# Optimization experiments

Measured on AMD Instinct MI355X. Metric: run time of the kernel, lower is better.

Reference implementation:

```python
import jax, jax.numpy as jnp
import numpy as np

N = 65536   # number of GP locations
M = 64      # max ancestor set size (contiguous window A(i) = {i-M+1..i})
B = 16384   # minibatch size


def setup_inputs() -> dict:
    rng = np.random.default_rng(0)
    i = np.arange(N)
    # CSR row lengths: U (lower-tri) row i has cols {max(0,i-M+1)..i}; V (upper-tri) row j has cols {j..min(j+M-1,N-1)}
    row_len_u = np.minimum(i + 1, M)
    row_len_v = np.minimum(M, N - i)
    crow_u = np.concatenate([[0], np.cumsum(row_len_u)]).astype(np.int32)
    crow_v = np.concatenate([[0], np.cumsum(row_len_v)]).astype(np.int32)
    nnz = int(crow_u[-1])  # 4192288, same for both matrices
    # off-diagonals small, diagonals near 1 (kept positive for logDet and solve stability)
    U_values = (rng.standard_normal(nnz) * 0.1).astype(np.float32)
    U_values[crow_u[1:] - 1] = rng.uniform(0.8, 1.2, N).astype(np.float32)  # last entry of row i = (i,i)
    V_values = (rng.standard_normal(nnz) * 0.1).astype(np.float32)
    V_values[crow_v[:-1]] = rng.uniform(0.8, 1.2, N).astype(np.float32)    # first entry of row i = (i,i)
    mean = (rng.standard_normal(N) * 0.5).astype(np.float32)
    mean_post = (rng.standard_normal(N) * 0.5).astype(np.float32)
    y = rng.standard_normal(N).astype(np.float32)
    mini_indices = rng.integers(0, N, B).astype(np.int32)
    return {
        'U_values': jnp.asarray(U_values),
        'V_values': jnp.asarray(V_values),
        'mean': jnp.asarray(mean),
        'mean_post': jnp.asarray(mean_post),
        'y': jnp.asarray(y),
        'noise': jnp.float32(0.1),
        'mini_indices': jnp.asarray(mini_indices),
        'crow_u': jnp.asarray(crow_u),
        'crow_v': jnp.asarray(crow_v),
    }


def reference(U_values, V_values, mean, mean_post, y, noise, mini_indices, crow_u, crow_v):
    nnz = U_values.shape[0]
    g = mini_indices                       # [B] selected rows
    L = jnp.minimum(g + 1, M)              # n_anc per selected row
    p = jnp.arange(M)
    valid = p[None, :] >= (M - L)[:, None]                 # [B,M] right-aligned validity mask
    anc = g[:, None] - (M - 1 - p)[None, :]                # global ancestor index at padded slot p
    anc_c = jnp.clip(anc, 0, N - 1)

    # get_sub_rows(UTrans): row g entries at A(g), right-aligned into [B,M]
    u_idx = crow_u[g][:, None] + (p[None, :] - (M - L)[:, None])
    U_sub = jnp.where(valid, U_values[jnp.clip(u_idx, 0, nnz - 1)], 0.0)

    # ragged mean difference gather (masked scatter in the original)
    md = jnp.where(valid, (mean - mean_post)[anc_c], 0.0)  # [B,M]

    # get_sub_mat(V, unit_diag=True): V[A(g),A(g)] bottom-right aligned, identity padding
    jrow = anc_c[:, :, None]                               # global row index of block row r
    icol = anc_c[:, None, :]                               # global col index of block col c
    vidx = crow_v[jrow] + (icol - jrow)                    # CSR value index of V[jrow, icol]
    blk_mask = (valid[:, :, None] & valid[:, None, :]
                & (p[None, :, None] <= p[None, None, :]))  # upper-tri of active block
    eye = jnp.eye(M, dtype=U_values.dtype)
    V_sub = jnp.where(blk_mask, V_values[jnp.clip(vidx, 0, nnz - 1)], eye[None, :, :])  # [B,M,M]

    # batched triangular solves
    ej = jnp.zeros((B, M), U_values.dtype).at[:, -1].set(1.0)
    sol_e = jax.scipy.linalg.solve_triangular(V_sub, ej[:, :, None], lower=False)
    marginalVarPost = jnp.sum(sol_e * sol_e, axis=(1, 2))  # [B]
    sol_u = jax.scipy.linalg.solve_triangular(V_sub, U_sub[:, :, None], lower=False)
    innerCov = -0.5 * jnp.sum(sol_u * sol_u)

    innerMean = -0.5 * jnp.sum(jnp.sum(U_sub * md, axis=1) ** 2)

    # log-determinant terms from diagonal gathers
    logDet = (jnp.sum(jnp.log(U_values[crow_u[g + 1] - 1]))
              - jnp.sum(jnp.log(V_values[crow_v[g]])))

    # Gaussian expected likelihood (noise is not None branch)
    resid = y[g] - mean_post[g]
    ell = (-0.5 * B * jnp.log(2.0 * jnp.pi * noise)
           - (jnp.sum(resid * resid) + jnp.sum(marginalVarPost)) / (2.0 * noise))

    return logDet + innerMean + innerCov + ell
```

## Files before the change

kernel.cpp:

```cpp
#include <hip/hip_runtime.h>
#include <math.h>

constexpr int kN = 65536;
constexpr int kB = 16384;
constexpr int kTileW = 2560;

static __device__ __forceinline__ float bcastf(float v, int lane) {
    union { float f; int i; } u;
    u.f = v;
    u.i = __builtin_amdgcn_readlane(u.i, lane);
    return u.f;
}

static __device__ __forceinline__ void gload_lds16(const float* g, float* l) {
    __builtin_amdgcn_global_load_lds(
        (const __attribute__((address_space(1))) void*)g,
        (__attribute__((address_space(3))) void*)l, 16, 0, 0);
}
static __device__ __forceinline__ void gload_lds4(const float* g, float* l) {
    __builtin_amdgcn_global_load_lds(
        (const __attribute__((address_space(1))) void*)g,
        (__attribute__((address_space(3))) void*)l, 4, 0, 0);
}

static __device__ __forceinline__ int row_start(int j) {
    const int t = j >> 4;
    return 1024 * t - 128 * t * (t - 1) + (64 - 16 * t) * (j - 16 * t);
}

static __device__ __forceinline__ bool is_hot(int g) {
    return (g >= 63) && (g <= kN - 63);
}

__global__ __launch_bounds__(64) void gp_solve_kernel(
    const float* __restrict__ Uv,
    const float* __restrict__ Vv,
    const float* __restrict__ mean,
    const float* __restrict__ mean_post,
    const float* __restrict__ y,
    const int*   __restrict__ gidx,
    const int*   __restrict__ crow_u,
    const int*   __restrict__ crow_v,
    const float* __restrict__ noise,
    float*       __restrict__ partial)
{
    __shared__ __align__(16) float myl[kTileW];

    const int lane = (int)threadIdx.x;
    const int b    = (int)blockIdx.x;
    const int g    = gidx[b];

    const int  anc = g - 63 + lane;
    const bool vl  = (anc >= 0);

    const int L  = (g + 1 < 64) ? (g + 1) : 64;
    const int ub = (g >= 63) ? (2016 + 64 * (g - 63)) : crow_u[g];

    float uval = 0.0f, md = 0.0f;
    if (vl) {
        uval = Uv[ub + lane - (64 - L)];
        md   = mean[anc] - mean_post[anc];
    }
    const float yg  = y[g];
    const float mpg = mean_post[g];

    if (is_hot(g)) {
        const float* base = Vv + 64 * (g - 63);
        {
            const float* src = base + 4 * lane;
            #pragma unroll
            for (int k = 0; k < 4; ++k)
                gload_lds16(src + 256 * k, myl + 256 * k);
        }
        #pragma unroll
        for (int k = 0; k < 3; ++k) {
            const int w   = 256 * k + 4 * lane;
            const int jj  = ((w >> 4) * 171) >> 9;
            const int col = w - 48 * jj;
            gload_lds16(base + 64 * (16 + jj) + col, myl + 1024 + 256 * k);
        }
        #pragma unroll
        for (int k = 0; k < 2; ++k) {
            const int w = 256 * k + 4 * lane;
            gload_lds16(base + 64 * (32 + (w >> 5)) + (w & 31), myl + 1792 + 256 * k);
        }
        {
            const int w = 4 * lane;
            gload_lds16(base + 64 * (48 + (w >> 4)) + (w & 15), myl + 2304);
        }
    } else {
        int rowbase = 0;
        if (vl) rowbase = crow_v[anc];
        for (int j = 0; j < 64; ++j) {
            const int rbj = __builtin_amdgcn_readlane(rowbase, j);
            const int dst = row_start(j);
            if (lane < 64 - j) {
                if (g - 63 + j >= 0)
                    gload_lds4(Vv + rbj + lane, myl + dst);
                else
                    myl[dst + lane] = 0.0f;
            }
        }
    }
    asm volatile("s_waitcnt vmcnt(0) lgkmcnt(0)" ::: "memory");

    const int rs = row_start(lane);
    const float d0   = myl[rs];
    const float diag = vl ? d0 : 1.0f;
    const float invd = 1.0f / diag;

    const float* vrow = myl + (rs - lane);
    float v[64];
    #pragma unroll
    for (int i = 0; i < 64; i += 2) {
        const float a0 = vrow[i];
        const float a1 = vrow[i + 1];
        v[i]     = a0 * invd;
        v[i + 1] = a1 * invd;
    }

    float r_e = (lane == 63) ? invd : 0.0f;
    float r_u = uval * invd;
    float acc_e = 0.0f, acc_u = 0.0f;

    #pragma unroll
    for (int i = 63; i >= 0; --i) {
        const float s_e = bcastf(r_e, i);
        const float s_u = bcastf(r_u, i);
        r_e = fmaf(-v[i], s_e, r_e);
        r_u = fmaf(-v[i], s_u, r_u);
        acc_e = fmaf(s_e, s_e, acc_e);
        acc_u = fmaf(s_u, s_u, acc_u);
    }

    float dot = uval * md;
    #pragma unroll
    for (int m = 1; m < 64; m <<= 1)
        dot += __shfl_xor(dot, m, 64);

    const float ulast  = bcastf(uval, 63);
    const float vfirst = bcastf(diag, 63);

    if (lane == 0) {
        const float resid = yg - mpg;
        const float inv2n = 0.5f / noise[0];
        partial[b] = __logf(ulast) - __logf(vfirst)
                   - 0.5f * dot * dot
                   - 0.5f * acc_u
                   - (resid * resid + acc_e) * inv2n;
    }
}

__global__ __launch_bounds__(1024) void gp_reduce_kernel(
    const float* __restrict__ partial,
    const float* __restrict__ noise,
    float*       __restrict__ out)
{
    __shared__ float ws[16];
    const int t = (int)threadIdx.x;
    float a = 0.0f;
    #pragma unroll
    for (int k = 0; k < 4; ++k) {
        const float4 p = reinterpret_cast<const float4*>(partial)[t + 1024 * k];
        a += (p.x + p.y) + (p.z + p.w);
    }
    #pragma unroll
    for (int m = 1; m < 64; m <<= 1)
        a += __shfl_xor(a, m, 64);
    if ((t & 63) == 0) ws[t >> 6] = a;
    __syncthreads();
    if (t == 0) {
        float tot = 0.0f;
        #pragma unroll
        for (int k = 0; k < 16; ++k) tot += ws[k];
        tot += -0.5f * (float)kB * logf(2.0f * 3.14159265358979323846f * noise[0]);
        out[0] = tot;
    }
}

extern "C" void kernel_launch(void* const* d_in, const int* in_sizes, int n_in,
                              void* d_out, int out_size, void* d_ws, size_t ws_size,
                              hipStream_t stream)
{
    const float* Uv        = (const float*)d_in[0];
    const float* Vv        = (const float*)d_in[1];
    const float* mean      = (const float*)d_in[2];
    const float* mean_post = (const float*)d_in[3];
    const float* y         = (const float*)d_in[4];
    const float* noise     = (const float*)d_in[5];
    const int*   gidx      = (const int*)d_in[6];
    const int*   crow_u    = (const int*)d_in[7];
    const int*   crow_v    = (const int*)d_in[8];
    float* partial = (float*)d_ws;

    gp_solve_kernel<<<dim3(kB), dim3(64), 0, stream>>>(
        Uv, Vv, mean, mean_post, y, gidx, crow_u, crow_v, noise, partial);
    gp_reduce_kernel<<<dim3(1), dim3(1024), 0, stream>>>(
        partial, noise, (float*)d_out);
}
```

Baseline: 36.94 us.

## Bucket-sort minibatch rows and swizzle block order for L2 locality

Adds a counting sort of the minibatch indices into 1024 buckets of 64 rows each, using a histogram, a scan and an atomic scatter. The solve kernel then reads its row from the sorted order, with a block-id swizzle that spreads contiguous sorted ranges across the 8 XCDs. The goal is for blocks whose V windows overlap to run close together on the same XCD so those V tile loads hit in L2. The cost is four extra small kernel launches and their atomics. Because the scatter order is nondeterministic, the summation order of the partials also becomes nondeterministic.

```diff
diff --git a/kernel.cpp b/kernel.cpp
--- a/kernel.cpp
+++ b/kernel.cpp
@@ -4,6 +4,7 @@
 constexpr int kN = 65536;
 constexpr int kB = 16384;
 constexpr int kTileW = 2560;
+constexpr int kBuckets = 1024;
 
 static __device__ __forceinline__ float bcastf(float v, int lane) {
     union { float f; int i; } u;
@@ -31,6 +32,50 @@
 static __device__ __forceinline__ bool is_hot(int g) {
     return (g >= 63) && (g <= kN - 63);
 }
+
+
+__global__ __launch_bounds__(1024) void gp_zero_hist(int* __restrict__ hist) {
+    hist[threadIdx.x] = 0;
+}
+
+__global__ __launch_bounds__(1024) void gp_hist_kernel(
+    const int* __restrict__ gidx, int* __restrict__ hist)
+{
+    const int i = (int)blockIdx.x * 1024 + (int)threadIdx.x;
+    atomicAdd(&hist[gidx[i] >> 6], 1);
+}
+
+__global__ __launch_bounds__(1024) void gp_scan_kernel(
+    const int* __restrict__ hist, int* __restrict__ base)
+{
+    __shared__ int wsum[16];
+    const int t = (int)threadIdx.x, lane = t & 63, w = t >> 6;
+    const int v = hist[t];
+    int x = v;
+    #pragma unroll
+    for (int d = 1; d < 64; d <<= 1) {
+        const int n = __shfl_up(x, d, 64);
+        if (lane >= d) x += n;
+    }
+    if (lane == 63) wsum[w] = x;
+    __syncthreads();
+    if (t == 0) {
+        int acc = 0;
+        #pragma unroll
+        for (int k = 0; k < 16; ++k) { const int s = wsum[k]; wsum[k] = acc; acc += s; }
+    }
+    __syncthreads();
+    base[t] = x - v + wsum[w];
+}
+
+__global__ __launch_bounds__(1024) void gp_scatter_kernel(
+    const int* __restrict__ gidx, int* __restrict__ base, int* __restrict__ sorted)
+{
+    const int i = (int)blockIdx.x * 1024 + (int)threadIdx.x;
+    const int pos = atomicAdd(&base[gidx[i] >> 6], 1);
+    sorted[pos] = i;
+}
+
 
 __global__ __launch_bounds__(64) void gp_solve_kernel(
     const float* __restrict__ Uv,
@@ -42,12 +87,15 @@
     const int*   __restrict__ crow_u,
     const int*   __restrict__ crow_v,
     const float* __restrict__ noise,
+    const int*   __restrict__ sorted,
     float*       __restrict__ partial)
 {
     __shared__ __align__(16) float myl[kTileW];
 
     const int lane = (int)threadIdx.x;
-    const int b    = (int)blockIdx.x;
+    const int bid  = (int)blockIdx.x;
+    const int slot = ((bid & 7) << 11) | (bid >> 3);
+    const int b    = sorted[slot];
     const int g    = gidx[b];
 
     const int  anc = g - 63 + lane;
@@ -144,10 +192,10 @@
     if (lane == 0) {
         const float resid = yg - mpg;
         const float inv2n = 0.5f / noise[0];
-        partial[b] = __logf(ulast) - __logf(vfirst)
-                   - 0.5f * dot * dot
-                   - 0.5f * acc_u
-                   - (resid * resid + acc_e) * inv2n;
+        partial[slot] = __logf(ulast) - __logf(vfirst)
+                      - 0.5f * dot * dot
+                      - 0.5f * acc_u
+                      - (resid * resid + acc_e) * inv2n;
     }
 }
 
@@ -191,10 +239,20 @@
     const int*   gidx      = (const int*)d_in[6];
     const int*   crow_u    = (const int*)d_in[7];
     const int*   crow_v    = (const int*)d_in[8];
-    float* partial = (float*)d_ws;
+
+    int*   ws_i    = (int*)d_ws;
+    int*   sorted  = ws_i;
+    int*   hist    = ws_i + kB;
+    int*   base    = ws_i + kB + kBuckets;
+    float* partial = (float*)(ws_i + kB + 2 * kBuckets);
+
+    gp_zero_hist   <<<dim3(1),       dim3(1024), 0, stream>>>(hist);
+    gp_hist_kernel <<<dim3(kB/1024), dim3(1024), 0, stream>>>(gidx, hist);
+    gp_scan_kernel <<<dim3(1),       dim3(1024), 0, stream>>>(hist, base);
+    gp_scatter_kernel<<<dim3(kB/1024), dim3(1024), 0, stream>>>(gidx, base, sorted);
 
     gp_solve_kernel<<<dim3(kB), dim3(64), 0, stream>>>(
-        Uv, Vv, mean, mean_post, y, gidx, crow_u, crow_v, noise, partial);
+        Uv, Vv, mean, mean_post, y, gidx, crow_u, crow_v, noise, sorted, partial);
     gp_reduce_kernel<<<dim3(1), dim3(1024), 0, stream>>>(
         partial, noise, (float*)d_out);
 }
```

Measured after the change: 48.15 us. 30.3% more time.

## Process eight samples per wave with double-buffered LDS prefetch

Applied to the files above, without the earlier changes.

Each 64-thread block now handles eight minibatch rows instead of one. It uses two LDS buffers so the async global-to-LDS load of the next sample's V block, U row and means overlaps the triangular solve of the current one, with partial vmcnt waits on the hot path. This cuts block count and launch overhead, hides memory latency inside a wave, and makes the final reduction read one float4 per thread. The trade-off is less parallelism across blocks (2048 waves), more LDS per block, and correctness that depends on the hand-counted vmcnt(13) wait being right.

```diff
diff --git a/kernel.cpp b/kernel.cpp
--- a/kernel.cpp
+++ b/kernel.cpp
@@ -3,7 +3,13 @@
 
 constexpr int kN = 65536;
 constexpr int kB = 16384;
+constexpr int kEPB = 8;
+constexpr int kBlocks = kB / kEPB;
 constexpr int kTileW = 2560;
+constexpr int kAuxU = 2560;
+constexpr int kAuxM = 2624;
+constexpr int kAuxP = 2688;
+constexpr int kBufW = 2752;
 
 static __device__ __forceinline__ float bcastf(float v, int lane) {
     union { float f; int i; } u;
@@ -23,6 +29,8 @@
         (__attribute__((address_space(3))) void*)l, 4, 0, 0);
 }
 
+#define CB() asm volatile("" ::: "memory")
+
 static __device__ __forceinline__ int row_start(int j) {
     const int t = j >> 4;
     return 1024 * t - 128 * t * (t - 1) + (64 - 16 * t) * (j - 16 * t);
@@ -31,6 +39,123 @@
 static __device__ __forceinline__ bool is_hot(int g) {
     return (g >= 63) && (g <= kN - 63);
 }
+
+static __device__ __forceinline__ void stage_one(
+    int g, int lane, float* buf,
+    const float* __restrict__ Uv, const float* __restrict__ Vv,
+    const float* __restrict__ mean, const float* __restrict__ mean_post,
+    const int* __restrict__ crow_u, const int* __restrict__ crow_v)
+{
+    if (is_hot(g)) {
+        const float* base = Vv + 64 * (g - 63);
+        {
+            const float* src = base + 4 * lane;
+            #pragma unroll
+            for (int k = 0; k < 4; ++k)
+                gload_lds16(src + 256 * k, buf + 256 * k);
+        }
+        #pragma unroll
+        for (int k = 0; k < 3; ++k) {
+            const int w   = 256 * k + 4 * lane;
+            const int jj  = ((w >> 4) * 171) >> 9;
+            const int col = w - 48 * jj;
+            gload_lds16(base + 64 * (16 + jj) + col, buf + 1024 + 256 * k);
+        }
+        #pragma unroll
+        for (int k = 0; k < 2; ++k) {
+            const int w = 256 * k + 4 * lane;
+            gload_lds16(base + 64 * (32 + (w >> 5)) + (w & 31), buf + 1792 + 256 * k);
+        }
+        {
+            const int w = 4 * lane;
+            gload_lds16(base + 64 * (48 + (w >> 4)) + (w & 15), buf + 2304);
+        }
+        const int ub = 2016 + 64 * (g - 63);
+        gload_lds4(Uv + ub + lane,               buf + kAuxU);
+        gload_lds4(mean + (g - 63) + lane,       buf + kAuxM);
+        gload_lds4(mean_post + (g - 63) + lane,  buf + kAuxP);
+    } else {
+        const int  anc = g - 63 + lane;
+        const bool vl  = (anc >= 0);
+        const int  L   = (g + 1 < 64) ? (g + 1) : 64;
+        const int  ub  = crow_u[g];
+        for (int j = 0; j < 64; ++j) {
+            if ((g - 63 + j) < 0 && lane < 64 - j)
+                buf[row_start(j) + lane] = 0.0f;
+        }
+        buf[kAuxU + lane] = 0.0f;
+        buf[kAuxM + lane] = 0.0f;
+        buf[kAuxP + lane] = 0.0f;
+        asm volatile("s_waitcnt lgkmcnt(0)" ::: "memory");
+        int rowbase = 0;
+        if (vl) rowbase = crow_v[anc];
+        for (int j = 0; j < 64; ++j) {
+            const int rbj = __builtin_amdgcn_readlane(rowbase, j);
+            if ((g - 63 + j) >= 0 && lane < 64 - j)
+                gload_lds4(Vv + rbj + lane, buf + row_start(j));
+        }
+        if (vl) {
+            gload_lds4(Uv + ub + lane - (64 - L), buf + kAuxU);
+            gload_lds4(mean + anc,                buf + kAuxM);
+            gload_lds4(mean_post + anc,           buf + kAuxP);
+        }
+    }
+}
+
+static __device__ __forceinline__ float compute_one(
+    int g, int lane, const float* buf, float inv2n)
+{
+    const int  anc = g - 63 + lane;
+    const bool vl  = (anc >= 0);
+
+    const int rs = row_start(lane);
+    const float d0   = buf[rs];
+    const float diag = vl ? d0 : 1.0f;
+    const float invd = 1.0f / diag;
+
+    const float uval = buf[kAuxU + lane];
+    const float md   = buf[kAuxM + lane] - buf[kAuxP + lane];
+
+    const float* vrow = buf + (rs - lane);
+    float v[64];
+    #pragma unroll
+    for (int i = 0; i < 64; i += 2) {
+        const float a0 = vrow[i];
+        const float a1 = vrow[i + 1];
+        v[i]     = a0 * invd;
+        v[i + 1] = a1 * invd;
+    }
+
+    float r_e = (lane == 63) ? invd : 0.0f;
+    float r_u = uval * invd;
+    float acc_e = 0.0f, acc_u = 0.0f;
+
+    #pragma unroll
+    for (int i = 63; i >= 0; --i) {
+        const float s_e = bcastf(r_e, i);
+        const float s_u = bcastf(r_u, i);
+        r_e = fmaf(-v[i], s_e, r_e);
+        r_u = fmaf(-v[i], s_u, r_u);
+        acc_e = fmaf(s_e, s_e, acc_e);
+        acc_u = fmaf(s_u, s_u, acc_u);
+    }
+
+    float dot = uval * md;
+    #pragma unroll
+    for (int m = 1; m < 64; m <<= 1)
+        dot += __shfl_xor(dot, m, 64);
+
+    const float ulast  = bcastf(uval, 63);
+    const float vfirst = bcastf(diag, 63);
+
+    return __logf(ulast) - __logf(vfirst)
+         - 0.5f * dot * dot
+         - 0.5f * acc_u
+         - acc_e * inv2n;
+}
+
+#define WAIT_HOT()  asm volatile("s_waitcnt vmcnt(13) lgkmcnt(0)" ::: "memory")
+#define WAIT_ALL()  asm volatile("s_waitcnt vmcnt(0)  lgkmcnt(0)" ::: "memory")
 
 __global__ __launch_bounds__(64) void gp_solve_kernel(
     const float* __restrict__ Uv,
@@ -44,126 +169,70 @@
     const float* __restrict__ noise,
     float*       __restrict__ partial)
 {
-    __shared__ __align__(16) float myl[kTileW];
-
-    const int lane = (int)threadIdx.x;
-    const int b    = (int)blockIdx.x;
-    const int g    = gidx[b];
-
-    const int  anc = g - 63 + lane;
-    const bool vl  = (anc >= 0);
-
-    const int L  = (g + 1 < 64) ? (g + 1) : 64;
-    const int ub = (g >= 63) ? (2016 + 64 * (g - 63)) : crow_u[g];
-
-    float uval = 0.0f, md = 0.0f;
-    if (vl) {
-        uval = Uv[ub + lane - (64 - L)];
-        md   = mean[anc] - mean_post[anc];
-    }
-    const float yg  = y[g];
-    const float mpg = mean_post[g];
-
-    if (is_hot(g)) {
-        const float* base = Vv + 64 * (g - 63);
-        {
-            const float* src = base + 4 * lane;
-            #pragma unroll
-            for (int k = 0; k < 4; ++k)
-                gload_lds16(src + 256 * k, myl + 256 * k);
-        }
-        #pragma unroll
-        for (int k = 0; k < 3; ++k) {
-            const int w   = 256 * k + 4 * lane;
-            const int jj  = ((w >> 4) * 171) >> 9;
-            const int col = w - 48 * jj;
-            gload_lds16(base + 64 * (16 + jj) + col, myl + 1024 + 256 * k);
-        }
-        #pragma unroll
-        for (int k = 0; k < 2; ++k) {
-            const int w = 256 * k + 4 * lane;
-            gload_lds16(base + 64 * (32 + (w >> 5)) + (w & 31), myl + 1792 + 256 * k);
-        }
-        {
-            const int w = 4 * lane;
-            gload_lds16(base + 64 * (48 + (w >> 4)) + (w & 15), myl + 2304);
-        }
-    } else {
-        int rowbase = 0;
-        if (vl) rowbase = crow_v[anc];
-        for (int j = 0; j < 64; ++j) {
-            const int rbj = __builtin_amdgcn_readlane(rowbase, j);
-            const int dst = row_start(j);
-            if (lane < 64 - j) {
-                if (g - 63 + j >= 0)
-                    gload_lds4(Vv + rbj + lane, myl + dst);
-                else
-                    myl[dst + lane] = 0.0f;
-            }
-        }
-    }
-    asm volatile("s_waitcnt vmcnt(0) lgkmcnt(0)" ::: "memory");
-
-    const int rs = row_start(lane);
-    const float d0   = myl[rs];
-    const float diag = vl ? d0 : 1.0f;
-    const float invd = 1.0f / diag;
-
-    const float* vrow = myl + (rs - lane);
-    float v[64];
-    #pragma unroll
-    for (int i = 0; i < 64; i += 2) {
-        const float a0 = vrow[i];
-        const float a1 = vrow[i + 1];
-        v[i]     = a0 * invd;
-        v[i + 1] = a1 * invd;
-    }
-
-    float r_e = (lane == 63) ? invd : 0.0f;
-    float r_u = uval * invd;
-    float acc_e = 0.0f, acc_u = 0.0f;
-
-    #pragma unroll
-    for (int i = 63; i >= 0; --i) {
-        const float s_e = bcastf(r_e, i);
-        const float s_u = bcastf(r_u, i);
-        r_e = fmaf(-v[i], s_e, r_e);
-        r_u = fmaf(-v[i], s_u, r_u);
-        acc_e = fmaf(s_e, s_e, acc_e);
-        acc_u = fmaf(s_u, s_u, acc_u);
-    }
-
-    float dot = uval * md;
-    #pragma unroll
-    for (int m = 1; m < 64; m <<= 1)
-        dot += __shfl_xor(dot, m, 64);
-
-    const float ulast  = bcastf(uval, 63);
-    const float vfirst = bcastf(diag, 63);
-
-    if (lane == 0) {
-        const float resid = yg - mpg;
-        const float inv2n = 0.5f / noise[0];
-        partial[b] = __logf(ulast) - __logf(vfirst)
-                   - 0.5f * dot * dot
-                   - 0.5f * acc_u
-                   - (resid * resid + acc_e) * inv2n;
-    }
-}
-
-__global__ __launch_bounds__(1024) void gp_reduce_kernel(
+    __shared__ __align__(16) float bufA[kBufW];
+    __shared__ __align__(16) float bufB[kBufW];
+
+    const int lane  = (int)threadIdx.x;
+    const int bbase = (int)blockIdx.x * kEPB;
+
+    const int g0 = gidx[bbase + 0], g1 = gidx[bbase + 1];
+    const int g2 = gidx[bbase + 2], g3 = gidx[bbase + 3];
+    const int g4 = gidx[bbase + 4], g5 = gidx[bbase + 5];
+    const int g6 = gidx[bbase + 6], g7 = gidx[bbase + 7];
+    const float inv2n = 0.5f / noise[0];
+
+    float rsum = 0.0f;
+    {
+        const float r0 = y[g0] - mean_post[g0], r1 = y[g1] - mean_post[g1];
+        const float r2 = y[g2] - mean_post[g2], r3 = y[g3] - mean_post[g3];
+        const float r4 = y[g4] - mean_post[g4], r5 = y[g5] - mean_post[g5];
+        const float r6 = y[g6] - mean_post[g6], r7 = y[g7] - mean_post[g7];
+        rsum = ((r0 * r0 + r1 * r1) + (r2 * r2 + r3 * r3))
+             + ((r4 * r4 + r5 * r5) + (r6 * r6 + r7 * r7));
+    }
+    CB();
+
+    float accum = 0.0f;
+    int  gA = g0;
+    stage_one(gA, lane, bufA, Uv, Vv, mean, mean_post, crow_u, crow_v);
+    CB();
+
+    #pragma unroll 1
+    for (int ee = 0; ee < 4; ++ee) {
+        const int gB = (ee < 2) ? (ee == 0 ? g1 : g3) : (ee == 2 ? g5 : g7);
+        const bool hB = is_hot(gB);
+        stage_one(gB, lane, bufB, Uv, Vv, mean, mean_post, crow_u, crow_v);
+        CB();
+        if (hB) WAIT_HOT(); else WAIT_ALL();
+        accum += compute_one(gA, lane, bufA, inv2n);
+        CB();
+
+        int gC = 0; bool hC = false;
+        if (ee < 3) {
+            gC = (ee == 0) ? g2 : (ee == 1 ? g4 : g6);
+            hC = is_hot(gC);
+            stage_one(gC, lane, bufA, Uv, Vv, mean, mean_post, crow_u, crow_v);
+            CB();
+        }
+        if (ee < 3 && hC) WAIT_HOT(); else WAIT_ALL();
+        accum += compute_one(gB, lane, bufB, inv2n);
+        CB();
+        gA = gC;
+    }
+
+    if (lane == 0)
+        partial[blockIdx.x] = accum - rsum * inv2n;
+}
+
+__global__ __launch_bounds__(512) void gp_reduce_kernel(
     const float* __restrict__ partial,
     const float* __restrict__ noise,
     float*       __restrict__ out)
 {
-    __shared__ float ws[16];
+    __shared__ float ws[8];
     const int t = (int)threadIdx.x;
-    float a = 0.0f;
-    #pragma unroll
-    for (int k = 0; k < 4; ++k) {
-        const float4 p = reinterpret_cast<const float4*>(partial)[t + 1024 * k];
-        a += (p.x + p.y) + (p.z + p.w);
-    }
+    const float4 p = reinterpret_cast<const float4*>(partial)[t];
+    float a = (p.x + p.y) + (p.z + p.w);
     #pragma unroll
     for (int m = 1; m < 64; m <<= 1)
         a += __shfl_xor(a, m, 64);
@@ -172,7 +241,7 @@
     if (t == 0) {
         float tot = 0.0f;
         #pragma unroll
-        for (int k = 0; k < 16; ++k) tot += ws[k];
+        for (int k = 0; k < 8; ++k) tot += ws[k];
         tot += -0.5f * (float)kB * logf(2.0f * 3.14159265358979323846f * noise[0]);
         out[0] = tot;
     }
@@ -193,8 +262,8 @@
     const int*   crow_v    = (const int*)d_in[8];
     float* partial = (float*)d_ws;
 
-    gp_solve_kernel<<<dim3(kB), dim3(64), 0, stream>>>(
+    gp_solve_kernel<<<dim3(kBlocks), dim3(64), 0, stream>>>(
         Uv, Vv, mean, mean_post, y, gidx, crow_u, crow_v, noise, partial);
-    gp_reduce_kernel<<<dim3(1), dim3(1024), 0, stream>>>(
+    gp_reduce_kernel<<<dim3(1), dim3(512), 0, stream>>>(
         partial, noise, (float*)d_out);
 }
```

Result: slower. 62.55 us (+69.3%).

## Process four batch elements per block with software-pipelined LDS tile staging

Applied to the files above, without the earlier changes.

Each 64-thread block now handles four minibatch rows and accumulates their contributions in registers. After the current V tile has been copied from LDS into registers, the global-to-LDS load of the next row's tile is issued, so that load overlaps the triangular-solve compute. The partial-sum array shrinks fourfold and the reduce kernel reads one float4 per thread. In exchange, the grid has a quarter as many blocks, which reduces parallelism and wave-level latency hiding, and the LDS buffer is reused across iterations, relying on explicit waitcnt ordering.

```diff
diff --git a/kernel.cpp b/kernel.cpp
--- a/kernel.cpp
+++ b/kernel.cpp
@@ -3,6 +3,8 @@
 
 constexpr int kN = 65536;
 constexpr int kB = 16384;
+constexpr int kEPB = 4;
+constexpr int kBlocks = kB / kEPB;
 constexpr int kTileW = 2560;
 
 static __device__ __forceinline__ float bcastf(float v, int lane) {
@@ -30,6 +32,52 @@
 
 static __device__ __forceinline__ bool is_hot(int g) {
     return (g >= 63) && (g <= kN - 63);
+}
+
+static __device__ __forceinline__ void stage_tile(
+    int g, int lane, float* buf,
+    const float* __restrict__ Vv, const int* __restrict__ crow_v)
+{
+    if (is_hot(g)) {
+        const float* base = Vv + 64 * (g - 63);
+        {
+            const float* src = base + 4 * lane;
+            #pragma unroll
+            for (int k = 0; k < 4; ++k)
+                gload_lds16(src + 256 * k, buf + 256 * k);
+        }
+        #pragma unroll
+        for (int k = 0; k < 3; ++k) {
+            const int w   = 256 * k + 4 * lane;
+            const int jj  = ((w >> 4) * 171) >> 9;
+            const int col = w - 48 * jj;
+            gload_lds16(base + 64 * (16 + jj) + col, buf + 1024 + 256 * k);
+        }
+        #pragma unroll
+        for (int k = 0; k < 2; ++k) {
+            const int w = 256 * k + 4 * lane;
+            gload_lds16(base + 64 * (32 + (w >> 5)) + (w & 31), buf + 1792 + 256 * k);
+        }
+        {
+            const int w = 4 * lane;
+            gload_lds16(base + 64 * (48 + (w >> 4)) + (w & 15), buf + 2304);
+        }
+    } else {
+        const int  anc = g - 63 + lane;
+        const bool vl  = (anc >= 0);
+        for (int j = 0; j < 64; ++j) {
+            if ((g - 63 + j) < 0 && lane < 64 - j)
+                buf[row_start(j) + lane] = 0.0f;
+        }
+        asm volatile("s_waitcnt lgkmcnt(0)" ::: "memory");
+        int rowbase = 0;
+        if (vl) rowbase = crow_v[anc];
+        for (int j = 0; j < 64; ++j) {
+            const int rbj = __builtin_amdgcn_readlane(rowbase, j);
+            if ((g - 63 + j) >= 0 && lane < 64 - j)
+                gload_lds4(Vv + rbj + lane, buf + row_start(j));
+        }
+    }
 }
 
 __global__ __launch_bounds__(64) void gp_solve_kernel(
@@ -44,111 +92,82 @@
     const float* __restrict__ noise,
     float*       __restrict__ partial)
 {
-    __shared__ __align__(16) float myl[kTileW];
-
-    const int lane = (int)threadIdx.x;
-    const int b    = (int)blockIdx.x;
-    const int g    = gidx[b];
-
-    const int  anc = g - 63 + lane;
-    const bool vl  = (anc >= 0);
-
-    const int L  = (g + 1 < 64) ? (g + 1) : 64;
-    const int ub = (g >= 63) ? (2016 + 64 * (g - 63)) : crow_u[g];
-
-    float uval = 0.0f, md = 0.0f;
-    if (vl) {
-        uval = Uv[ub + lane - (64 - L)];
-        md   = mean[anc] - mean_post[anc];
+    __shared__ __align__(16) float buf[kTileW];
+    const int lane  = (int)threadIdx.x;
+    const int bbase = (int)blockIdx.x * kEPB;
+
+    const float inv2n = 0.5f / noise[0];
+    int gcur = gidx[bbase];
+    stage_tile(gcur, lane, buf, Vv, crow_v);
+    asm volatile("s_waitcnt vmcnt(0)" ::: "memory");
+
+    float accum = 0.0f;
+
+    #pragma unroll 1
+    for (int e = 0; e < kEPB; ++e) {
+        const int gnext = (e < kEPB - 1) ? gidx[bbase + e + 1] : 63;
+        const int  anc = gcur - 63 + lane;
+        const bool vl  = (anc >= 0);
+        const int  L   = (gcur + 1 < 64) ? (gcur + 1) : 64;
+        const int  ub  = (gcur >= 63) ? (2016 + 64 * (gcur - 63)) : crow_u[gcur];
+        float uval = 0.0f, md = 0.0f;
+        if (vl) {
+            uval = Uv[ub + lane - (64 - L)];
+            md   = mean[anc] - mean_post[anc];
+        }
+        const float yv  = y[gcur];
+        const float mpv = mean_post[gcur];
+
+        const int rs = row_start(lane);
+        const float d0   = buf[rs];
+        const float diag = vl ? d0 : 1.0f;
+        const float invd = 1.0f / diag;
+        const float* vrow = buf + (rs - lane);
+        float v[64];
+        #pragma unroll
+        for (int i = 0; i < 64; i += 2) {
+            const float a0 = vrow[i];
+            const float a1 = vrow[i + 1];
+            v[i]     = a0 * invd;
+            v[i + 1] = a1 * invd;
+        }
+        asm volatile("s_waitcnt lgkmcnt(0)" ::: "memory");
+        if (e < kEPB - 1)
+            stage_tile(gnext, lane, buf, Vv, crow_v);
+        __builtin_amdgcn_sched_barrier(0);
+
+        float r_e = (lane == 63) ? invd : 0.0f;
+        float r_u = uval * invd;
+        float acc_e = 0.0f, acc_u = 0.0f;
+        #pragma unroll
+        for (int i = 63; i >= 0; --i) {
+            const float s_e = bcastf(r_e, i);
+            const float s_u = bcastf(r_u, i);
+            r_e = fmaf(-v[i], s_e, r_e);
+            r_u = fmaf(-v[i], s_u, r_u);
+            acc_e = fmaf(s_e, s_e, acc_e);
+            acc_u = fmaf(s_u, s_u, acc_u);
+        }
+
+        float dot = uval * md;
+        #pragma unroll
+        for (int m = 1; m < 64; m <<= 1)
+            dot += __shfl_xor(dot, m, 64);
+
+        const float ulast  = bcastf(uval, 63);
+        const float vfirst = bcastf(diag, 63);
+        const float resid  = yv - mpv;
+        accum += __logf(ulast) - __logf(vfirst)
+               - 0.5f * dot * dot
+               - 0.5f * acc_u
+               - (resid * resid + acc_e) * inv2n;
+
+        asm volatile("s_waitcnt vmcnt(0)" ::: "memory");
+        gcur = gnext;
     }
-    const float yg  = y[g];
-    const float mpg = mean_post[g];
-
-    if (is_hot(g)) {
-        const float* base = Vv + 64 * (g - 63);
-        {
-            const float* src = base + 4 * lane;
-            #pragma unroll
-            for (int k = 0; k < 4; ++k)
-                gload_lds16(src + 256 * k, myl + 256 * k);
-        }
-        #pragma unroll
-        for (int k = 0; k < 3; ++k) {
-            const int w   = 256 * k + 4 * lane;
-            const int jj  = ((w >> 4) * 171) >> 9;
-            const int col = w - 48 * jj;
-            gload_lds16(base + 64 * (16 + jj) + col, myl + 1024 + 256 * k);
-        }
-        #pragma unroll
-        for (int k = 0; k < 2; ++k) {
-            const int w = 256 * k + 4 * lane;
-            gload_lds16(base + 64 * (32 + (w >> 5)) + (w & 31), myl + 1792 + 256 * k);
-        }
-        {
-            const int w = 4 * lane;
-            gload_lds16(base + 64 * (48 + (w >> 4)) + (w & 15), myl + 2304);
-        }
-    } else {
-        int rowbase = 0;
-        if (vl) rowbase = crow_v[anc];
-        for (int j = 0; j < 64; ++j) {
-            const int rbj = __builtin_amdgcn_readlane(rowbase, j);
-            const int dst = row_start(j);
-            if (lane < 64 - j) {
-                if (g - 63 + j >= 0)
-                    gload_lds4(Vv + rbj + lane, myl + dst);
-                else
-                    myl[dst + lane] = 0.0f;
-            }
-        }
-    }
-    asm volatile("s_waitcnt vmcnt(0) lgkmcnt(0)" ::: "memory");
-
-    const int rs = row_start(lane);
-    const float d0   = myl[rs];
-    const float diag = vl ? d0 : 1.0f;
-    const float invd = 1.0f / diag;
-
-    const float* vrow = myl + (rs - lane);
-    float v[64];
-    #pragma unroll
-    for (int i = 0; i < 64; i += 2) {
-        const float a0 = vrow[i];
-        const float a1 = vrow[i + 1];
-        v[i]     = a0 * invd;
-        v[i + 1] = a1 * invd;
-    }
-
-    float r_e = (lane == 63) ? invd : 0.0f;
-    float r_u = uval * invd;
-    float acc_e = 0.0f, acc_u = 0.0f;
-
-    #pragma unroll
-    for (int i = 63; i >= 0; --i) {
-        const float s_e = bcastf(r_e, i);
-        const float s_u = bcastf(r_u, i);
-        r_e = fmaf(-v[i], s_e, r_e);
-        r_u = fmaf(-v[i], s_u, r_u);
-        acc_e = fmaf(s_e, s_e, acc_e);
-        acc_u = fmaf(s_u, s_u, acc_u);
-    }
-
-    float dot = uval * md;
-    #pragma unroll
-    for (int m = 1; m < 64; m <<= 1)
-        dot += __shfl_xor(dot, m, 64);
-
-    const float ulast  = bcastf(uval, 63);
-    const float vfirst = bcastf(diag, 63);
-
-    if (lane == 0) {
-        const float resid = yg - mpg;
-        const float inv2n = 0.5f / noise[0];
-        partial[b] = __logf(ulast) - __logf(vfirst)
-                   - 0.5f * dot * dot
-                   - 0.5f * acc_u
-                   - (resid * resid + acc_e) * inv2n;
-    }
+
+    if (lane == 0)
+        partial[blockIdx.x] = accum;
 }
 
 __global__ __launch_bounds__(1024) void gp_reduce_kernel(
@@ -158,12 +177,8 @@
 {
     __shared__ float ws[16];
     const int t = (int)threadIdx.x;
-    float a = 0.0f;
-    #pragma unroll
-    for (int k = 0; k < 4; ++k) {
-        const float4 p = reinterpret_cast<const float4*>(partial)[t + 1024 * k];
-        a += (p.x + p.y) + (p.z + p.w);
-    }
+    const float4 p = reinterpret_cast<const float4*>(partial)[t];
+    float a = (p.x + p.y) + (p.z + p.w);
     #pragma unroll
     for (int m = 1; m < 64; m <<= 1)
         a += __shfl_xor(a, m, 64);
@@ -193,7 +208,7 @@
     const int*   crow_v    = (const int*)d_in[8];
     float* partial = (float*)d_ws;
 
-    gp_solve_kernel<<<dim3(kB), dim3(64), 0, stream>>>(
+    gp_solve_kernel<<<dim3(kBlocks), dim3(64), 0, stream>>>(
         Uv, Vv, mean, mean_post, y, gidx, crow_u, crow_v, noise, partial);
     gp_reduce_kernel<<<dim3(1), dim3(1024), 0, stream>>>(
         partial, noise, (float*)d_out);
```

New measurement: 38.53 us. +4.3%, slower.
